# Kernel tuning notes

Measured on AMD Instinct MI355X. Metric: run time of the kernel, lower is better.

## Reference

```python
import jax, jax.numpy as jnp
import numpy as np

EMBED_DIM = 1024
NUM_HEADS = 16
HEAD_DIM = EMBED_DIM // NUM_HEADS


def setup_inputs() -> dict:
    key = jax.random.key(0)
    ks = jax.random.split(key, 9)
    s = 1.0 / np.sqrt(EMBED_DIM)
    X = jax.random.normal(ks[0], (4, 2048, EMBED_DIM), dtype=jnp.float32)
    # Linear weights stored as [in, out] for x @ W + b
    Wq = jax.random.uniform(ks[1], (EMBED_DIM, EMBED_DIM), jnp.float32, -s, s)
    bq = jax.random.uniform(ks[2], (EMBED_DIM,), jnp.float32, -s, s)
    Wk = jax.random.uniform(ks[3], (EMBED_DIM, EMBED_DIM), jnp.float32, -s, s)
    bk = jax.random.uniform(ks[4], (EMBED_DIM,), jnp.float32, -s, s)
    Wv = jax.random.uniform(ks[5], (EMBED_DIM, EMBED_DIM), jnp.float32, -s, s)
    bv = jax.random.uniform(ks[6], (EMBED_DIM,), jnp.float32, -s, s)
    Wo = jax.random.uniform(ks[7], (EMBED_DIM, EMBED_DIM), jnp.float32, -s, s)
    bo = jax.random.uniform(ks[8], (EMBED_DIM,), jnp.float32, -s, s)
    return {"X": X, "Wq": Wq, "bq": bq, "Wk": Wk, "bk": bk,
            "Wv": Wv, "bv": bv, "Wo": Wo, "bo": bo}


def reference(X, Wq, bq, Wk, bk, Wv, bv, Wo, bo):
    B, S, _ = X.shape
    def split_heads(t):  # [B,S,E] -> [B,H,S,D]
        return t.reshape(B, S, NUM_HEADS, HEAD_DIM).transpose(0, 2, 1, 3)
    Q = split_heads(X @ Wq + bq)
    K = split_heads(X @ Wk + bk)
    V = split_heads(X @ Wv + bv)
    scale = 1.0 / np.sqrt(HEAD_DIM).astype(np.float32)
    scores = jnp.einsum('bhqd,bhkd->bhqk', Q, K) * scale
    probs = jax.nn.softmax(scores, axis=-1)
    attn = jnp.einsum('bhqk,bhkd->bhqd', probs, V)  # [B,H,S,D]
    combined = attn.transpose(0, 2, 1, 3).reshape(B, S, EMBED_DIM)
    return combined @ Wo + bo
```

## Files before the change

kernel.cpp:

```cpp
#include <hip/hip_runtime.h>
#include <hip/hip_bf16.h>

#define EMBED 1024
#define NHEADS 16
#define HDIM 64
#define SEQ 2048
#define BATCH 4
#define ROWS (BATCH * SEQ)

typedef __attribute__((ext_vector_type(8))) short bf16x8;
typedef __attribute__((ext_vector_type(4))) float f32x4;
typedef __attribute__((ext_vector_type(2))) float f32x2;
typedef __attribute__((ext_vector_type(16))) float f32x16;
typedef __attribute__((ext_vector_type(4))) unsigned int u32x4;
typedef __attribute__((ext_vector_type(2))) unsigned int u32x2;
typedef __attribute__((ext_vector_type(2))) int i32x2;
typedef unsigned int u32;

#define SL2E 0.18033688011112042f

__device__ __forceinline__ short f2bf(float f) {
    u32 u = __builtin_bit_cast(u32, f) + 0x8000u;
    return (short)(u >> 16);
}

__device__ __forceinline__ u32 pkbf(float a, float b) {
    u32 ua = __builtin_bit_cast(u32, a) + 0x8000u;
    u32 ub = __builtin_bit_cast(u32, b) + 0x8000u;
    return __builtin_amdgcn_perm(ua, ub, 0x03020706u);
}

__device__ __forceinline__ float fexp2(float x) {
#if __has_builtin(__builtin_amdgcn_exp2f)
    return __builtin_amdgcn_exp2f(x);
#else
    return exp2f(x);
#endif
}

__device__ __forceinline__ void async16(const void* g, void* l) {
    __builtin_amdgcn_global_load_lds((const __attribute__((address_space(1))) u32*)g,
                                     (__attribute__((address_space(3))) u32*)l, 16, 0, 0);
}

__global__ __launch_bounds__(256) void convert_f32_bf16(const float* __restrict__ in,
                                                        short* __restrict__ out) {
    int i = (blockIdx.x * 256 + threadIdx.x) * 4;
    float4 v = *(const float4*)&in[i];
    u32x2 o = { pkbf(v.x, v.y), pkbf(v.z, v.w) };
    *(u32x2*)&out[i] = o;
}

__global__ __launch_bounds__(256) void transpose_w4(const float* __restrict__ W0,
                                                    const float* __restrict__ W1,
                                                    const float* __restrict__ W2,
                                                    const float* __restrict__ W3,
                                                    short* __restrict__ T0,
                                                    short* __restrict__ T1,
                                                    short* __restrict__ T2,
                                                    short* __restrict__ T3) {
    const int z = blockIdx.z;
    const float* W = (z == 0) ? W0 : (z == 1) ? W1 : (z == 2) ? W2 : W3;
    short* WT = (z == 0) ? T0 : (z == 1) ? T1 : (z == 2) ? T2 : T3;
    const float sc = (z == 0) ? SL2E : 1.0f;
    __shared__ float T[64][65];
    const int k0 = blockIdx.y * 64, n0 = blockIdx.x * 64;
    const int rr = threadIdx.x >> 4, cc = (threadIdx.x & 15) * 4;
    #pragma unroll
    for (int p = 0; p < 4; ++p) {
        int r = p * 16 + rr;
        float4 v = *(const float4*)&W[(size_t)(k0 + r) * EMBED + n0 + cc];
        T[r][cc] = v.x * sc; T[r][cc + 1] = v.y * sc; T[r][cc + 2] = v.z * sc; T[r][cc + 3] = v.w * sc;
    }
    __syncthreads();
    #pragma unroll
    for (int p = 0; p < 4; ++p) {
        int r = p * 16 + rr;
        u32x2 o = { pkbf(T[cc][r], T[cc + 1][r]), pkbf(T[cc + 2][r], T[cc + 3][r]) };
        *(u32x2*)&WT[(size_t)(n0 + r) * EMBED + k0 + cc] = o;
    }
}

__global__ __launch_bounds__(512, 2) void gemm_p128(const short* __restrict__ A,
                                                    const short* __restrict__ BT,
                                                    const float* __restrict__ b0,
                                                    const float* __restrict__ b1,
                                                    const float* __restrict__ b2,
                                                    void* __restrict__ C0,
                                                    void* __restrict__ C1,
                                                    void* __restrict__ C2,
                                                    int mode) {
    __shared__ short As[2][8192];
    __shared__ short Bs[2][16384];
    const int tid = threadIdx.x;
    const int lane = tid & 63;
    const int wid = tid >> 6;
    const int c16 = lane & 15, quad = lane >> 4, sw = c16 & 7;
    const int wm = wid >> 2, wn = wid & 3;
    const int gx = gridDim.x;
    const int hid = blockIdx.y * gx + blockIdx.x;
    const int cpx = (gx * gridDim.y) >> 3;
    const int tle = (hid & 7) * cpx + (hid >> 3);
    const int bx = tle % gx, by = tle / gx;
    const int rowblk = by * 128, colblk = bx * 256;

    const int r0 = tid >> 3;
    const int g0 = (tid & 7) ^ (r0 & 7);
    const short* aS0 = A + (size_t)(rowblk + r0) * EMBED + g0 * 8;
    const short* bS0 = BT + (size_t)(colblk + r0) * EMBED + g0 * 8;

#define STAGE_A(SBUF, V) do { \
    const short* _s = aS0 + (V) * 64; \
    async16(_s,         &As[SBUF][tid * 8]); \
    async16(_s + 65536, &As[SBUF][tid * 8 + 4096]); \
} while (0)
#define STAGE_B0(SBUF, V) do { \
    const short* _s = bS0 + (V) * 64; \
    async16(_s,         &Bs[SBUF][tid * 8]); \
    async16(_s + 65536, &Bs[SBUF][tid * 8 + 4096]); \
} while (0)
#define STAGE_B1(SBUF, V) do { \
    const short* _s = bS0 + 131072 + (V) * 64; \
    async16(_s,         &Bs[SBUF][tid * 8 + 8192]); \
    async16(_s + 65536, &Bs[SBUF][tid * 8 + 12288]); \
} while (0)

    f32x4 acc[4][4] = {};
    bf16x8 aU[2][2], bE[2][2], bO[2][2];

#define LDA(BUF, MH) do { \
    _Pragma("unroll") \
    for (int fm = 0; fm < 2; ++fm) { \
        const int row = wm * 64 + (MH) * 32 + fm * 16 + c16; \
        _Pragma("unroll") \
        for (int ks = 0; ks < 2; ++ks) \
            aU[fm][ks] = *(const bf16x8*)&As[BUF][row * 64 + ((ks * 4 + quad) ^ sw) * 8]; \
    } \
} while (0)
#define LDB(BUF, NH, DST) do { \
    _Pragma("unroll") \
    for (int fn = 0; fn < 2; ++fn) { \
        const int col = wn * 64 + (NH) * 32 + fn * 16 + c16; \
        _Pragma("unroll") \
        for (int ks = 0; ks < 2; ++ks) \
            DST[fn][ks] = *(const bf16x8*)&Bs[BUF][col * 64 + ((ks * 4 + quad) ^ sw) * 8]; \
    } \
} while (0)
#define MM(MB, NB, BM_) do { \
    _Pragma("unroll") \
    for (int fm = 0; fm < 2; ++fm) \
        _Pragma("unroll") \
        for (int fn = 0; fn < 2; ++fn) \
            _Pragma("unroll") \
            for (int ks = 0; ks < 2; ++ks) \
                acc[(MB) + fm][(NB) + fn] = \
                    __builtin_amdgcn_mfma_f32_16x16x32_bf16(aU[fm][ks], BM_[fn][ks], \
                        acc[(MB) + fm][(NB) + fn], 0, 0, 0); \
} while (0)
#define PH_MID() do { \
    __builtin_amdgcn_s_barrier(); \
    asm volatile("s_waitcnt lgkmcnt(0)" ::: "memory"); \
    __builtin_amdgcn_s_setprio(1); \
} while (0)
#define PH_END(VM) do { \
    __builtin_amdgcn_s_setprio(0); \
    if (VM) asm volatile("s_waitcnt vmcnt(6)" ::: "memory"); \
    __builtin_amdgcn_s_barrier(); \
} while (0)

    STAGE_B0(0, 0); STAGE_A(0, 0); STAGE_B1(0, 0);
    STAGE_B0(1, 1); STAGE_A(1, 1); STAGE_B1(1, 1);
    asm volatile("s_waitcnt vmcnt(6)" ::: "memory");
    __builtin_amdgcn_s_barrier();

    #pragma unroll 1
    for (int it = 0; it < 8; ++it) {
        const int u = 2 * it;
        const int v2 = (u + 2) & 15, v3 = (u + 3) & 15;
        LDA(0, 0); LDB(0, 0, bE);                     PH_MID(); MM(0, 0, bE); PH_END(0);
        LDB(0, 1, bO);            STAGE_B0(0, v2);    PH_MID(); MM(0, 2, bO); PH_END(0);
        LDA(0, 1);                STAGE_B1(0, v2);    PH_MID(); MM(2, 2, bO); PH_END(0);
                 STAGE_A(0, v2);     PH_MID(); MM(2, 0, bE); PH_END(1);
        LDA(1, 0); LDB(1, 0, bE);                     PH_MID(); MM(0, 0, bE); PH_END(0);
        LDB(1, 1, bO);            STAGE_B0(1, v3);    PH_MID(); MM(0, 2, bO); PH_END(0);
        LDA(1, 1);                STAGE_B1(1, v3);    PH_MID(); MM(2, 2, bO); PH_END(0);
                 STAGE_A(1, v3);     PH_MID(); MM(2, 0, bE); PH_END(1);
    }

    asm volatile("s_waitcnt vmcnt(0)" ::: "memory");

    const int rb0 = rowblk + wm * 64 + quad * 4;
    const int cb0 = wn * 64 + c16;
    if (mode == 0) {
        const int z = colblk >> 10;
        const int cm = colblk & 1023;
        const float* bias = (z == 0) ? b0 : (z == 1) ? b1 : b2;
        if (z == 2) {
            short* Vt = (short*)C2;
            #pragma unroll
            for (int m = 0; m < 4; ++m) {
                const int row = rb0 + (m >> 1) * 32 + (m & 1) * 16;
                const int b = row >> 11, s = row & 2047;
                #pragma unroll
                for (int n = 0; n < 4; ++n) {
                    const int cv = cm + cb0 + (n >> 1) * 32 + (n & 1) * 16;
                    const int head = cv >> 6, d = cv & 63;
                    const float bv = bias[cv];
                    u32x2 o = { pkbf(acc[m][n][0] + bv, acc[m][n][1] + bv),
                                pkbf(acc[m][n][2] + bv, acc[m][n][3] + bv) };
                    *(u32x2*)&Vt[((size_t)(b * NHEADS + head) * HDIM + d) * SEQ + s] = o;
                }
            }
        } else {
            short* Cq = (short*)((z == 0) ? C0 : C1);
            const float bsc = (z == 0) ? SL2E : 1.0f;
            #pragma unroll
            for (int m = 0; m < 4; ++m) {
                const int row = rb0 + (m >> 1) * 32 + (m & 1) * 16;
                #pragma unroll
                for (int n = 0; n < 4; ++n) {
                    const int col = cm + cb0 + (n >> 1) * 32 + (n & 1) * 16;
                    const float bv = bias[col] * bsc;
                    #pragma unroll
                    for (int r = 0; r < 4; ++r)
                        Cq[(size_t)(row + r) * EMBED + col] = f2bf(acc[m][n][r] + bv);
                }
            }
        }
    } else {
        float* Co = (float*)C0;
        #pragma unroll
        for (int m = 0; m < 4; ++m) {
            const int row = rb0 + (m >> 1) * 32 + (m & 1) * 16;
            #pragma unroll
            for (int n = 0; n < 4; ++n) {
                const int col = colblk + cb0 + (n >> 1) * 32 + (n & 1) * 16;
                const float bv = b0[col];
                #pragma unroll
                for (int r = 0; r < 4; ++r)
                    Co[(size_t)(row + r) * EMBED + col] = acc[m][n][r] + bv;
            }
        }
    }
#undef PH_END
#undef PH_MID
#undef MM
#undef LDB
#undef LDA
#undef STAGE_B1
#undef STAGE_B0
#undef STAGE_A
}

__global__ __launch_bounds__(256, 3) void attn_mfma(const short* __restrict__ Qb,
                                                    const short* __restrict__ Kb,
                                                    const short* __restrict__ Vt,
                                                    short* __restrict__ Ob) {
    __shared__ short SH[16384];
    const int tid = threadIdx.x;
    const int wave = tid >> 6, lane = tid & 63;
    const int l31 = lane & 31, h = lane >> 5;
    const int swz = l31 & 7;
    const int hid = blockIdx.y * 16 + blockIdx.x;
    const int tle = (hid & 7) * 128 + (hid >> 3);
    const int qb = tle & 15, bh = tle >> 4;
    const int b = bh >> 4, hd = bh & 15;
    const size_t base = (size_t)b * SEQ * EMBED + (size_t)hd * HDIM;
    const size_t vbase = (size_t)bh * HDIM * SEQ;
    const int q0 = qb * 128;

    bf16x8 qf[4];
    #pragma unroll
    for (int ks = 0; ks < 4; ++ks)
        qf[ks] = *(const bf16x8*)&Qb[base + (size_t)(q0 + wave * 32 + l31) * EMBED + ks * 16 + h * 8];

    const short* kp[2];
    const short* vp[2];
    int ldofs[2];
    #pragma unroll
    for (int it = 0; it < 2; ++it) {
        int ci = (it * 4 + wave) * 64 + lane;
        int row = ci >> 3, g = (ci & 7) ^ (row & 7);
        kp[it] = Kb + base + (size_t)row * EMBED + g * 8;
        vp[it] = Vt + vbase + (size_t)row * SEQ + g * 8;
        ldofs[it] = (it * 4 + wave) * 512;
    }

    f32x16 O[2] = {};
    f32x2 ls = {0.0f, 0.0f};

    #pragma unroll
    for (int it = 0; it < 2; ++it) {
        async16(kp[it], &SH[ldofs[it]]);
        async16(vp[it], &SH[8192 + ldofs[it]]);
        kp[it] += 64 * EMBED;
        vp[it] += 64;
    }
    asm volatile("s_waitcnt vmcnt(0)" ::: "memory");
    __builtin_amdgcn_s_barrier();

    #pragma unroll 2
    for (int kt = 0; kt < SEQ / 64; ++kt) {
        const int bo = (kt & 1) * 4096;
        const short* Ks = SH + bo;
        const short* Vs = SH + 8192 + bo;
        if (kt < SEQ / 64 - 1) {
            const int nbo = 4096 - bo;
            #pragma unroll
            for (int it = 0; it < 2; ++it) {
                async16(kp[it], &SH[nbo + ldofs[it]]);
                async16(vp[it], &SH[8192 + nbo + ldofs[it]]);
                kp[it] += 64 * EMBED;
                vp[it] += 64;
            }
        }

        f32x16 st[2] = {};
        __builtin_amdgcn_s_setprio(1);
        #pragma unroll
        for (int nt = 0; nt < 2; ++nt)
            #pragma unroll
            for (int ks = 0; ks < 4; ++ks) {
                bf16x8 ak = *(const bf16x8*)&Ks[(nt * 32 + l31) * 64 + ((ks * 2 + h) ^ swz) * 8];
                st[nt] = __builtin_amdgcn_mfma_f32_32x32x16_bf16(ak, qf[ks], st[nt], 0, 0, 0);
            }
        __builtin_amdgcn_s_setprio(0);

        u32 pk[2][8];
        #pragma unroll
        for (int nt = 0; nt < 2; ++nt)
            #pragma unroll
            for (int i = 0; i < 8; ++i) {
                float e0 = fexp2(st[nt][2 * i]), e1 = fexp2(st[nt][2 * i + 1]);
                f32x2 e = { e0, e1 };
                ls += e;
                pk[nt][i] = pkbf(e0, e1);
            }

        __builtin_amdgcn_s_setprio(1);
        #pragma unroll
        for (int ks = 0; ks < 4; ++ks) {
            const int nt = ks >> 1, bs = (ks & 1) * 4;
            u32x4 fr;
#if __has_builtin(__builtin_amdgcn_permlane32_swap)
            i32x2 sA = __builtin_amdgcn_permlane32_swap((int)pk[nt][bs + 0], (int)pk[nt][bs + 2], false, false);
            i32x2 sB = __builtin_amdgcn_permlane32_swap((int)pk[nt][bs + 1], (int)pk[nt][bs + 3], false, false);
            fr.x = (u32)sA.x; fr.y = (u32)sB.x; fr.z = (u32)sA.y; fr.w = (u32)sB.y;
#else
            u32 s0 = h ? pk[nt][bs + 0] : pk[nt][bs + 2];
            u32 s1 = h ? pk[nt][bs + 1] : pk[nt][bs + 3];
            u32 r0 = (u32)__shfl_xor((int)s0, 32);
            u32 r1 = (u32)__shfl_xor((int)s1, 32);
            fr.x = h ? r0 : pk[nt][bs + 0];
            fr.y = h ? r1 : pk[nt][bs + 1];
            fr.z = h ? pk[nt][bs + 2] : r0;
            fr.w = h ? pk[nt][bs + 3] : r1;
#endif
            bf16x8 pf = __builtin_bit_cast(bf16x8, fr);
            #pragma unroll
            for (int mt = 0; mt < 2; ++mt) {
                bf16x8 vf = *(const bf16x8*)&Vs[(mt * 32 + l31) * 64 + ((ks * 2 + h) ^ swz) * 8];
                O[mt] = __builtin_amdgcn_mfma_f32_32x32x16_bf16(vf, pf, O[mt], 0, 0, 0);
            }
        }
        __builtin_amdgcn_s_setprio(0);

        asm volatile("s_waitcnt vmcnt(0)" ::: "memory");
        __builtin_amdgcn_s_barrier();
    }

    float lsum = ls.x + ls.y;
    lsum += __shfl_xor(lsum, 32);
    float inv = 1.0f / lsum;

    const int wbase = wave * 2048;
    #pragma unroll
    for (int mt = 0; mt < 2; ++mt)
        #pragma unroll
        for (int m = 0; m < 4; ++m) {
            u32x2 wv;
            wv.x = pkbf(O[mt][4 * m + 0] * inv, O[mt][4 * m + 1] * inv);
            wv.y = pkbf(O[mt][4 * m + 2] * inv, O[mt][4 * m + 3] * inv);
            int u = mt * 8 + 2 * m + h;
            int su = u ^ ((l31 & 7) << 1);
            *(u32x2*)&SH[wbase + l31 * 64 + su * 4] = wv;
        }
    __syncthreads();
    #pragma unroll
    for (int p = 0; p < 4; ++p) {
        int ci = p * 256 + tid;
        int wq = ci >> 8, rem = ci & 255;
        int r = rem >> 3, cch = rem & 7;
        int su = (2 * cch) ^ ((r & 7) << 1);
        bf16x8 val = *(const bf16x8*)&SH[wq * 2048 + r * 64 + su * 4];
        *(bf16x8*)&Ob[base + (size_t)(q0 + wq * 32 + r) * EMBED + cch * 8] = val;
    }
}

extern "C" void kernel_launch(void* const* d_in, const int* in_sizes, int n_in,
                              void* d_out, int out_size, void* d_ws, size_t ws_size,
                              hipStream_t stream)
{
    const float* X  = (const float*)d_in[0];
    const float* Wq = (const float*)d_in[1];
    const float* bq = (const float*)d_in[2];
    const float* Wk = (const float*)d_in[3];
    const float* bk = (const float*)d_in[4];
    const float* Wv = (const float*)d_in[5];
    const float* bv = (const float*)d_in[6];
    const float* Wo = (const float*)d_in[7];
    const float* bo = (const float*)d_in[8];
    float* out = (float*)d_out;

    const size_t NE = (size_t)ROWS * EMBED;
    short* Xbf = (short*)d_ws;
    short* Qb  = Xbf + NE;
    short* Kb  = Qb + NE;
    short* Vtb = Kb + NE;
    short* WqT = Vtb + NE;
    short* WkT = WqT + (size_t)EMBED * EMBED;
    short* WvT = WkT + (size_t)EMBED * EMBED;
    short* WoT = WvT + (size_t)EMBED * EMBED;

    convert_f32_bf16<<<(ROWS * EMBED) / 1024, 256, 0, stream>>>(X, Xbf);
    dim3 gw(16, 16, 4);
    transpose_w4<<<gw, 256, 0, stream>>>(Wq, Wk, Wv, Wo, WqT, WkT, WvT, WoT);

    dim3 gq(12, 64, 1);
    gemm_p128<<<gq, 512, 0, stream>>>(Xbf, WqT, bq, bk, bv, Qb, Kb, Vtb, 0);

    dim3 gt(SEQ / 128, BATCH * NHEADS);
    attn_mfma<<<gt, 256, 0, stream>>>(Qb, Kb, Vtb, Qb);

    dim3 gg(4, 64, 1);
    gemm_p128<<<gg, 512, 0, stream>>>(Qb, WoT, bo, bo, bo, out, out, out, 1);
}
```

Before: 277.1 us.

## Software-pipeline attention loop so next tile's QK overlaps current softmax and PV

```diff
diff --git a/kernel.cpp b/kernel.cpp
--- a/kernel.cpp
+++ b/kernel.cpp
@@ -286,88 +286,86 @@
         ldofs[it] = (it * 4 + wave) * 512;
     }
 
+#define STAGE_K(J) do { \
+    async16(kp[0], &SH[(J) * 4096 + ldofs[0]]); \
+    async16(kp[1], &SH[(J) * 4096 + ldofs[1]]); \
+    kp[0] += 64 * EMBED; kp[1] += 64 * EMBED; \
+} while (0)
+#define STAGE_V(J) do { \
+    async16(vp[0], &SH[8192 + (J) * 4096 + ldofs[0]]); \
+    async16(vp[1], &SH[8192 + (J) * 4096 + ldofs[1]]); \
+    vp[0] += 64; vp[1] += 64; \
+} while (0)
+#define QK_INTO(ST, J) do { \
+    _Pragma("unroll") \
+    for (int _z = 0; _z < 16; ++_z) { ST[0][_z] = 0.0f; ST[1][_z] = 0.0f; } \
+    __builtin_amdgcn_s_setprio(1); \
+    _Pragma("unroll") \
+    for (int nt = 0; nt < 2; ++nt) \
+        _Pragma("unroll") \
+        for (int ks = 0; ks < 4; ++ks) { \
+            bf16x8 ak = *(const bf16x8*)&SH[(J) * 4096 + (nt * 32 + l31) * 64 + ((ks * 2 + h) ^ swz) * 8]; \
+            ST[nt] = __builtin_amdgcn_mfma_f32_32x32x16_bf16(ak, qf[ks], ST[nt], 0, 0, 0); \
+        } \
+    __builtin_amdgcn_s_setprio(0); \
+} while (0)
+
     f32x16 O[2] = {};
+    f32x16 stA[2], stB[2];
     f32x2 ls = {0.0f, 0.0f};
 
-    #pragma unroll
-    for (int it = 0; it < 2; ++it) {
-        async16(kp[it], &SH[ldofs[it]]);
-        async16(vp[it], &SH[8192 + ldofs[it]]);
-        kp[it] += 64 * EMBED;
-        vp[it] += 64;
-    }
+    STAGE_K(0); STAGE_V(0); STAGE_K(1);
     asm volatile("s_waitcnt vmcnt(0)" ::: "memory");
     __builtin_amdgcn_s_barrier();
-
-    #pragma unroll 2
-    for (int kt = 0; kt < SEQ / 64; ++kt) {
-        const int bo = (kt & 1) * 4096;
-        const short* Ks = SH + bo;
-        const short* Vs = SH + 8192 + bo;
-        if (kt < SEQ / 64 - 1) {
-            const int nbo = 4096 - bo;
-            #pragma unroll
-            for (int it = 0; it < 2; ++it) {
-                async16(kp[it], &SH[nbo + ldofs[it]]);
-                async16(vp[it], &SH[8192 + nbo + ldofs[it]]);
-                kp[it] += 64 * EMBED;
-                vp[it] += 64;
-            }
-        }
-
-        f32x16 st[2] = {};
-        __builtin_amdgcn_s_setprio(1);
-        #pragma unroll
-        for (int nt = 0; nt < 2; ++nt)
-            #pragma unroll
-            for (int ks = 0; ks < 4; ++ks) {
-                bf16x8 ak = *(const bf16x8*)&Ks[(nt * 32 + l31) * 64 + ((ks * 2 + h) ^ swz) * 8];
-                st[nt] = __builtin_amdgcn_mfma_f32_32x32x16_bf16(ak, qf[ks], st[nt], 0, 0, 0);
-            }
-        __builtin_amdgcn_s_setprio(0);
-
-        u32 pk[2][8];
-        #pragma unroll
-        for (int nt = 0; nt < 2; ++nt)
-            #pragma unroll
-            for (int i = 0; i < 8; ++i) {
-                float e0 = fexp2(st[nt][2 * i]), e1 = fexp2(st[nt][2 * i + 1]);
-                f32x2 e = { e0, e1 };
-                ls += e;
-                pk[nt][i] = pkbf(e0, e1);
-            }
-
-        __builtin_amdgcn_s_setprio(1);
-        #pragma unroll
-        for (int ks = 0; ks < 4; ++ks) {
-            const int nt = ks >> 1, bs = (ks & 1) * 4;
-            u32x4 fr;
-#if __has_builtin(__builtin_amdgcn_permlane32_swap)
-            i32x2 sA = __builtin_amdgcn_permlane32_swap((int)pk[nt][bs + 0], (int)pk[nt][bs + 2], false, false);
-            i32x2 sB = __builtin_amdgcn_permlane32_swap((int)pk[nt][bs + 1], (int)pk[nt][bs + 3], false, false);
-            fr.x = (u32)sA.x; fr.y = (u32)sB.x; fr.z = (u32)sA.y; fr.w = (u32)sB.y;
-#else
-            u32 s0 = h ? pk[nt][bs + 0] : pk[nt][bs + 2];
-            u32 s1 = h ? pk[nt][bs + 1] : pk[nt][bs + 3];
-            u32 r0 = (u32)__shfl_xor((int)s0, 32);
-            u32 r1 = (u32)__shfl_xor((int)s1, 32);
-            fr.x = h ? r0 : pk[nt][bs + 0];
-            fr.y = h ? r1 : pk[nt][bs + 1];
-            fr.z = h ? pk[nt][bs + 2] : r0;
-            fr.w = h ? pk[nt][bs + 3] : r1;
-#endif
-            bf16x8 pf = __builtin_bit_cast(bf16x8, fr);
-            #pragma unroll
-            for (int mt = 0; mt < 2; ++mt) {
-                bf16x8 vf = *(const bf16x8*)&Vs[(mt * 32 + l31) * 64 + ((ks * 2 + h) ^ swz) * 8];
-                O[mt] = __builtin_amdgcn_mfma_f32_32x32x16_bf16(vf, pf, O[mt], 0, 0, 0);
-            }
-        }
-        __builtin_amdgcn_s_setprio(0);
-
-        asm volatile("s_waitcnt vmcnt(0)" ::: "memory");
-        __builtin_amdgcn_s_barrier();
-    }
+    QK_INTO(stA, 0);
+    __builtin_amdgcn_s_barrier();
+
+#define ATT_BODY(CUR, NXT, STC, STN, DO_K, DO_V, DO_QK) do { \
+    if (DO_K) STAGE_K(CUR); \
+    if (DO_V) STAGE_V(NXT); \
+    if (DO_QK) QK_INTO(STN, NXT); \
+    u32 pk[2][8]; \
+    _Pragma("unroll") \
+    for (int nt = 0; nt < 2; ++nt) \
+        _Pragma("unroll") \
+        for (int i = 0; i < 8; ++i) { \
+            float e0 = fexp2(STC[nt][2 * i]), e1 = fexp2(STC[nt][2 * i + 1]); \
+            f32x2 e = { e0, e1 }; \
+            ls += e; \
+            pk[nt][i] = pkbf(e0, e1); \
+        } \
+    __builtin_amdgcn_s_setprio(1); \
+    _Pragma("unroll") \
+    for (int ks = 0; ks < 4; ++ks) { \
+        const int nt = ks >> 1, bs = (ks & 1) * 4; \
+        u32x4 fr; \
+        i32x2 sA = __builtin_amdgcn_permlane32_swap((int)pk[nt][bs + 0], (int)pk[nt][bs + 2], false, false); \
+        i32x2 sB = __builtin_amdgcn_permlane32_swap((int)pk[nt][bs + 1], (int)pk[nt][bs + 3], false, false); \
+        fr.x = (u32)sA.x; fr.y = (u32)sB.x; fr.z = (u32)sA.y; fr.w = (u32)sB.y; \
+        bf16x8 pf = __builtin_bit_cast(bf16x8, fr); \
+        _Pragma("unroll") \
+        for (int mt = 0; mt < 2; ++mt) { \
+            bf16x8 vf = *(const bf16x8*)&SH[8192 + (CUR) * 4096 + (mt * 32 + l31) * 64 + ((ks * 2 + h) ^ swz) * 8]; \
+            O[mt] = __builtin_amdgcn_mfma_f32_32x32x16_bf16(vf, pf, O[mt], 0, 0, 0); \
+        } \
+    } \
+    __builtin_amdgcn_s_setprio(0); \
+    asm volatile("s_waitcnt vmcnt(0)" ::: "memory"); \
+    __builtin_amdgcn_s_barrier(); \
+} while (0)
+
+    #pragma unroll 1
+    for (int t = 0; t < 30; t += 2) {
+        ATT_BODY(0, 1, stA, stB, 1, 1, 1);
+        ATT_BODY(1, 0, stB, stA, 1, 1, 1);
+    }
+    ATT_BODY(0, 1, stA, stB, 0, 1, 1);
+    ATT_BODY(1, 0, stB, stA, 0, 0, 0);
+
+#undef ATT_BODY
+#undef QK_INTO
+#undef STAGE_V
+#undef STAGE_K
 
     float lsum = ls.x + ls.y;
     lsum += __shfl_xor(lsum, 32);
```

Result: faster. 270.0 us (-2.5%).
